# Performance work log

Measured on AMD Instinct MI355X. Metric: run time of the kernel, lower is better.

The kernel has to match this reference:

```python
import jax, jax.numpy as jnp
import numpy as np


def setup_inputs() -> dict:
    key = jax.random.key(0)
    k1, k2 = jax.random.split(key)
    B, H, W = 64, 512, 512
    return {
        "output": jax.random.normal(k1, (B, H, W), dtype=jnp.float32),
        "target": jax.random.normal(k2, (B, H, W), dtype=jnp.float32),
        "patch_size": 8,
    }


def reference(output, target, patch_size):
    B, H, W = output.shape
    p = patch_size
    nh, nw = H // p, W // p  # torch.unfold drops any remainder
    def patches(x):
        # [B,H,W] -> [B, nh*nw, p*p], row-major over (i, j) like the nested loop
        x = x[:, : nh * p, : nw * p]
        x = x.reshape(B, nh, p, nw, p).transpose(0, 1, 3, 2, 4)
        return x.reshape(B, nh * nw, p * p)
    op = patches(output)
    tp = patches(target)
    # per-patch L1 loss (mean reduction) and per-patch mean of target
    losses = jnp.mean(jnp.abs(op - tp), axis=-1)  # [B, nh*nw]
    means = jnp.mean(tp, axis=-1)                 # [B, nh*nw]
    agree = jnp.argmax(losses, axis=-1) == jnp.argmax(means, axis=-1)  # [B]
    num_true = jnp.sum(agree).astype(jnp.int32)
    total_num = jnp.int32(B)
    num_false = total_num - num_true
    correctness = num_true.astype(jnp.float32) / total_num.astype(jnp.float32)
    return (total_num, num_true, num_false, correctness)
```

## Files before the change

kernel.cpp:

```cpp
#include <hip/hip_runtime.h>


__global__ void patch_sums_kernel(const float* __restrict__ outp,
                                  const float* __restrict__ tgt,
                                  float* __restrict__ losses,
                                  float* __restrict__ means) {
    const int bid = blockIdx.x;
    const int b   = bid >> 6;
    const int ph  = bid & 63;
    const int t   = threadIdx.x;

    const int col4  = t & 127;
    const int rbase = t >> 7;

    const size_t base = ((size_t)b * 512 + (size_t)ph * 8) * 512;

    float sAbs = 0.f, sT = 0.f;
#pragma unroll
    for (int k = 0; k < 4; ++k) {
        const int r = rbase + 2 * k;
        const size_t off = base + (size_t)r * 512 + (size_t)col4 * 4;
        const float4 o  = *reinterpret_cast<const float4*>(outp + off);
        const float4 tg = *reinterpret_cast<const float4*>(tgt  + off);
        sAbs += fabsf(o.x - tg.x) + fabsf(o.y - tg.y)
              + fabsf(o.z - tg.z) + fabsf(o.w - tg.w);
        sT   += tg.x + tg.y + tg.z + tg.w;
    }

    __shared__ float sA[256];
    __shared__ float sM[256];
    sA[t] = sAbs;
    sM[t] = sT;
    __syncthreads();

    if (t < 64) {
        const int i0 = 2 * t, i1 = 2 * t + 1, i2 = 128 + 2 * t, i3 = 129 + 2 * t;
        const float la = sA[i0] + sA[i1] + sA[i2] + sA[i3];
        const float lm = sM[i0] + sM[i1] + sM[i2] + sM[i3];
        const int g = b * 4096 + ph * 64 + t;
        losses[g] = la;
        means[g]  = lm;
    }
}

__global__ void batch_argmax_kernel(const float* __restrict__ losses,
                                    const float* __restrict__ means,
                                    int* __restrict__ agree) {
    const int b = blockIdx.x;
    const int t = threadIdx.x;
    const float* L = losses + (size_t)b * 4096;
    const float* M = means  + (size_t)b * 4096;

    float bl = -INFINITY, bm = -INFINITY;
    int il = 0x7fffffff, im = 0x7fffffff;
    for (int i = t; i < 4096; i += 256) {
        const float v = L[i];
        if (v > bl) { bl = v; il = i; }
        const float w = M[i];
        if (w > bm) { bm = w; im = i; }
    }

    __shared__ float svL[256]; __shared__ int siL[256];
    __shared__ float svM[256]; __shared__ int siM[256];
    svL[t] = bl; siL[t] = il; svM[t] = bm; siM[t] = im;
    __syncthreads();

    for (int s = 128; s > 0; s >>= 1) {
        if (t < s) {
            if (svL[t + s] > svL[t] || (svL[t + s] == svL[t] && siL[t + s] < siL[t])) {
                svL[t] = svL[t + s]; siL[t] = siL[t + s];
            }
            if (svM[t + s] > svM[t] || (svM[t + s] == svM[t] && siM[t + s] < siM[t])) {
                svM[t] = svM[t + s]; siM[t] = siM[t + s];
            }
        }
        __syncthreads();
    }

    if (t == 0) agree[b] = (siL[0] == siM[0]) ? 1 : 0;
}

__global__ void finalize_kernel(const int* __restrict__ agree,
                                float* __restrict__ outp) {
    const int t = threadIdx.x;
    int v = agree[t];
#pragma unroll
    for (int s = 32; s > 0; s >>= 1) v += __shfl_down(v, s);
    if (t == 0) {
        const float nt = (float)v;
        outp[0] = 64.0f;
        outp[1] = nt;
        outp[2] = 64.0f - nt;
        outp[3] = nt / 64.0f;
    }
}

extern "C" void kernel_launch(void* const* d_in, const int* in_sizes, int n_in,
                              void* d_out, int out_size, void* d_ws, size_t ws_size,
                              hipStream_t stream) {
    const float* outp = (const float*)d_in[0];
    const float* tgt  = (const float*)d_in[1];

    float* losses = (float*)d_ws;
    float* means  = losses + 64 * 4096;
    int*   agree  = (int*)(means + 64 * 4096);

    patch_sums_kernel<<<64 * 64, 256, 0, stream>>>(outp, tgt, losses, means);
    batch_argmax_kernel<<<64, 256, 0, stream>>>(losses, means, agree);
    finalize_kernel<<<1, 64, 0, stream>>>(agree, (float*)d_out);
}
```

Baseline: 32.87 us.

## Fuse per-batch argmax into patch-sum kernel via packed 64-bit atomicMax

Each block now reduces its 64 patch sums to a local argmax with wavefront shuffles. It then publishes the value and index as an order-preserving packed 64-bit key through atomicMax. This removes the separate batch argmax kernel and the round trip through intermediate loss and mean arrays, leaving a memset, the main kernel and a tiny finalize. It adds 64 contended atomics per batch entry and a memset launch, and it relies on the inverted-index packing to keep the lowest-index tie-break.

```diff
diff --git a/kernel.cpp b/kernel.cpp
--- a/kernel.cpp
+++ b/kernel.cpp
@@ -1,10 +1,15 @@
 #include <hip/hip_runtime.h>
 
 
+__device__ __forceinline__ unsigned ordf(float f) {
+    unsigned u = __float_as_uint(f);
+    return u ^ ((u >> 31) ? 0xFFFFFFFFu : 0x80000000u);
+}
+
 __global__ void patch_sums_kernel(const float* __restrict__ outp,
                                   const float* __restrict__ tgt,
-                                  float* __restrict__ losses,
-                                  float* __restrict__ means) {
+                                  unsigned long long* __restrict__ packedL,
+                                  unsigned long long* __restrict__ packedM) {
     const int bid = blockIdx.x;
     const int b   = bid >> 6;
     const int ph  = bid & 63;
@@ -35,55 +40,39 @@
 
     if (t < 64) {
         const int i0 = 2 * t, i1 = 2 * t + 1, i2 = 128 + 2 * t, i3 = 129 + 2 * t;
-        const float la = sA[i0] + sA[i1] + sA[i2] + sA[i3];
-        const float lm = sM[i0] + sM[i1] + sM[i2] + sM[i3];
-        const int g = b * 4096 + ph * 64 + t;
-        losses[g] = la;
-        means[g]  = lm;
+        float la = sA[i0] + sA[i1] + sA[i2] + sA[i3];
+        float lm = sM[i0] + sM[i1] + sM[i2] + sM[i3];
+        int   il = ph * 64 + t;
+        int   im = il;
+
+#pragma unroll
+        for (int s = 32; s > 0; s >>= 1) {
+            const float ol = __shfl_xor(la, s);
+            const int   oi = __shfl_xor(il, s);
+            if (ol > la || (ol == la && oi < il)) { la = ol; il = oi; }
+            const float om = __shfl_xor(lm, s);
+            const int   oj = __shfl_xor(im, s);
+            if (om > lm || (om == lm && oj < im)) { lm = om; im = oj; }
+        }
+
+        if (t == 0) {
+            const unsigned long long kl =
+                ((unsigned long long)ordf(la) << 32) | (unsigned)(4095 - il);
+            const unsigned long long km =
+                ((unsigned long long)ordf(lm) << 32) | (unsigned)(4095 - im);
+            atomicMax(&packedL[b], kl);
+            atomicMax(&packedM[b], km);
+        }
     }
 }
 
-__global__ void batch_argmax_kernel(const float* __restrict__ losses,
-                                    const float* __restrict__ means,
-                                    int* __restrict__ agree) {
-    const int b = blockIdx.x;
-    const int t = threadIdx.x;
-    const float* L = losses + (size_t)b * 4096;
-    const float* M = means  + (size_t)b * 4096;
-
-    float bl = -INFINITY, bm = -INFINITY;
-    int il = 0x7fffffff, im = 0x7fffffff;
-    for (int i = t; i < 4096; i += 256) {
-        const float v = L[i];
-        if (v > bl) { bl = v; il = i; }
-        const float w = M[i];
-        if (w > bm) { bm = w; im = i; }
-    }
-
-    __shared__ float svL[256]; __shared__ int siL[256];
-    __shared__ float svM[256]; __shared__ int siM[256];
-    svL[t] = bl; siL[t] = il; svM[t] = bm; siM[t] = im;
-    __syncthreads();
-
-    for (int s = 128; s > 0; s >>= 1) {
-        if (t < s) {
-            if (svL[t + s] > svL[t] || (svL[t + s] == svL[t] && siL[t + s] < siL[t])) {
-                svL[t] = svL[t + s]; siL[t] = siL[t + s];
-            }
-            if (svM[t + s] > svM[t] || (svM[t + s] == svM[t] && siM[t + s] < siM[t])) {
-                svM[t] = svM[t + s]; siM[t] = siM[t + s];
-            }
-        }
-        __syncthreads();
-    }
-
-    if (t == 0) agree[b] = (siL[0] == siM[0]) ? 1 : 0;
-}
-
-__global__ void finalize_kernel(const int* __restrict__ agree,
+__global__ void finalize_kernel(const unsigned long long* __restrict__ packedL,
+                                const unsigned long long* __restrict__ packedM,
                                 float* __restrict__ outp) {
     const int t = threadIdx.x;
-    int v = agree[t];
+    const unsigned il = (unsigned)(packedL[t] & 0xFFFFFFFFu);
+    const unsigned im = (unsigned)(packedM[t] & 0xFFFFFFFFu);
+    int v = (il == im) ? 1 : 0;
 #pragma unroll
     for (int s = 32; s > 0; s >>= 1) v += __shfl_down(v, s);
     if (t == 0) {
@@ -101,11 +90,11 @@
     const float* outp = (const float*)d_in[0];
     const float* tgt  = (const float*)d_in[1];
 
-    float* losses = (float*)d_ws;
-    float* means  = losses + 64 * 4096;
-    int*   agree  = (int*)(means + 64 * 4096);
+    unsigned long long* packedL = (unsigned long long*)d_ws;
+    unsigned long long* packedM = packedL + 64;
 
-    patch_sums_kernel<<<64 * 64, 256, 0, stream>>>(outp, tgt, losses, means);
-    batch_argmax_kernel<<<64, 256, 0, stream>>>(losses, means, agree);
-    finalize_kernel<<<1, 64, 0, stream>>>(agree, (float*)d_out);
+    hipMemsetAsync(d_ws, 0, 128 * sizeof(unsigned long long), stream);
+
+    patch_sums_kernel<<<64 * 64, 256, 0, stream>>>(outp, tgt, packedL, packedM);
+    finalize_kernel<<<1, 64, 0, stream>>>(packedL, packedM, (float*)d_out);
 }
```

Result: slower. 37.68 us (+14.6%).
